# Performance work log

Hardware: AMD Instinct MI355X
Metric: run time of the kernel (lower is better)

## Reference

```python
import jax, jax.numpy as jnp
import numpy as np

H, D, HID = 32, 128, 4096
I = H * D  # inner_dim = 4096
EPS = 1e-6

def l2norm(x):
    n = jnp.sqrt(jnp.sum(x * x, axis=-1, keepdims=True))
    return x / jnp.maximum(n, EPS)

def setup_inputs() -> dict:
    key = jax.random.key(0)
    ks = jax.random.split(key, 13)
    s = 0.02
    return {
        "hidden_states": jax.random.normal(ks[0], (1, 1, HID), jnp.float32),
        "rnn_state": jax.random.normal(ks[1], (1, H, D, D), jnp.float32),
        "conv_state": jax.random.normal(ks[2], (1, 3 * I, 3), jnp.float32),
        "W_qkv": (jax.random.normal(ks[3], (3 * I, HID), jnp.float32) * s),
        "W_z": (jax.random.normal(ks[4], (I, HID), jnp.float32) * s),
        "W_a": (jax.random.normal(ks[5], (H, HID), jnp.float32) * s),
        "W_b": (jax.random.normal(ks[6], (H, HID), jnp.float32) * s),
        "conv_w": (jax.random.normal(ks[7], (3 * I, 4), jnp.float32) * 0.2),  # depthwise kernel [C,1,4] squeezed
        "conv_b": jnp.zeros((3 * I,), jnp.float32),
        "A_log": jnp.log(jax.random.uniform(ks[8], (H,), jnp.float32, 0.5, 2.0)),
        "dt_bias": (jax.random.normal(ks[9], (H,), jnp.float32) * 0.1),
        "norm_w": jnp.ones((D,), jnp.float32),
        "W_out": (jax.random.normal(ks[10], (HID, I), jnp.float32) * s),
    }

def reference(hidden_states, rnn_state, conv_state, W_qkv, W_z, W_a, W_b,
              conv_w, conv_b, A_log, dt_bias, norm_w, W_out):
    B = hidden_states.shape[0]  # == 1 (enforced by original module's view)
    # QKV projection: [B,1,3I]
    qkv = jnp.einsum('bsh,ch->bsc', hidden_states, W_qkv)
    # depthwise causal conv over window of 4 (3 cached + 1 new)
    x_in = jnp.swapaxes(qkv, 1, 2)                      # [B,3I,1]
    conv_input = jnp.concatenate([conv_state, x_in], axis=2)  # [B,3I,4]
    new_conv_state = conv_input[:, :, 1:]
    y = jnp.einsum('bck,ck->bc', conv_input, conv_w) + conv_b
    y = jax.nn.silu(y)                                  # [B,3I]
    q, k, v = jnp.split(y, 3, axis=-1)
    q = q.reshape(B, H, D); k = k.reshape(B, H, D); v = v.reshape(B, H, D)
    # gating projections
    z = jnp.einsum('bsh,ch->bsc', hidden_states, W_z)   # [B,1,I]
    beta = jax.nn.sigmoid(jnp.einsum('bsh,nh->bsn', hidden_states, W_b))[:, 0]  # [B,H]
    a = jnp.einsum('bsh,nh->bsn', hidden_states, W_a)[:, 0]                     # [B,H]
    g = -jnp.exp(A_log) * jax.nn.softplus(a + dt_bias)  # [B,H]
    qn = l2norm(q) * (1.0 / np.sqrt(D))
    kn = l2norm(k)
    # gated delta-rule state update on [B,H,D,D]
    state = rnn_state * jnp.exp(g)[:, :, None, None]
    kv_mem = jnp.einsum('bhde,bhd->bhe', state, kn)
    delta = (v - kv_mem) * beta[..., None]
    state = state + kn[..., None] * delta[:, :, None, :]
    core = jnp.einsum('bhde,bhd->bhe', state, qn)       # [B,H,D]
    # per-head RMSNorm over D (fp32)
    var = jnp.mean(core * core, axis=-1, keepdims=True)
    core = norm_w * (core * jax.lax.rsqrt(var + EPS))
    core = core.reshape(B, 1, I)
    out = jnp.einsum('bsc,hc->bsh', core * jax.nn.silu(z), W_out)
    return out, state, new_conv_state
```

## Files before the change

kernel.cpp:

```cpp
#include <hip/hip_runtime.h>
#include <math.h>

#define HID   4096
#define NH    32
#define D     128
#define I_    4096
#define QKV_ROWS 12288
#define TOTAL_ROWS 16448

#define WS_QKV   0
#define WS_Z     12288
#define WS_AB    16384
#define WS_VEC   16448

typedef float f4 __attribute__((ext_vector_type(4)));

__device__ __forceinline__ float wave_reduce(float x) {
    for (int off = 32; off > 0; off >>= 1) x += __shfl_down(x, off, 64);
    return x;
}

__global__ __launch_bounds__(256) void matvec_all(
    const float* __restrict__ h,
    const float* __restrict__ Wqkv, const float* __restrict__ Wz,
    const float* __restrict__ Wa,   const float* __restrict__ Wb,
    float* __restrict__ ws)
{
    const int wave = threadIdx.x >> 6;
    const int lane = threadIdx.x & 63;
    const int row  = blockIdx.x * 4 + wave;

    const float* W; float* out; int r;
    if (row < QKV_ROWS)          { W = Wqkv; r = row;             out = ws + WS_QKV; }
    else if (row < 16384)        { W = Wz;   r = row - 12288;     out = ws + WS_Z;   }
    else if (row < 16416)        { W = Wa;   r = row - 16384;     out = ws + WS_AB;  }
    else                         { W = Wb;   r = row - 16416;     out = ws + WS_AB + 32; }

    const f4* wrow = (const f4*)(W + (size_t)r * HID);
    const f4* hv   = (const f4*)h;

    float acc = 0.f;
    #pragma unroll
    for (int i = 0; i < 16; ++i) {
        const f4 wv = __builtin_nontemporal_load(wrow + lane + i * 64);
        const f4 hh = hv[lane + i * 64];
        acc = fmaf(wv.x, hh.x, acc);
        acc = fmaf(wv.y, hh.y, acc);
        acc = fmaf(wv.z, hh.z, acc);
        acc = fmaf(wv.w, hh.w, acc);
    }
    acc = wave_reduce(acc);
    if (lane == 0) out[r] = acc;
}

__global__ __launch_bounds__(1024) void head_fused(
    const float* __restrict__ ws_in,
    const float* __restrict__ rnn_state,
    const float* __restrict__ conv_state,
    const float* __restrict__ conv_w,
    const float* __restrict__ conv_b,
    const float* __restrict__ A_log, const float* __restrict__ dt_bias,
    const float* __restrict__ norm_w,
    float* __restrict__ state_out,
    float* __restrict__ ncs_out,
    float* __restrict__ vec_out)
{
    const int hd   = blockIdx.x;
    const int tid  = threadIdx.x;
    const int e    = tid & 127;
    const int dgrp = tid >> 7;
    const int d0   = dgrp * 16;

    __shared__ float sy[3][D];
    __shared__ float skn[D], sqn[D];
    __shared__ float pkv[8][D], pcq[8][D];
    __shared__ float pkq[8];
    __shared__ float sgb[2];
    __shared__ float snrm[2];
    __shared__ float sdelta[D], score[D];
    __shared__ float red[2];

    if (tid < 384) {
        const int j  = tid >> 7;
        const int e2 = tid & 127;
        const int c  = j * I_ + hd * D + e2;
        const float* cs = conv_state + (size_t)c * 3;
        const f4 cw = *(const f4*)(conv_w + (size_t)c * 4);
        const float cs0 = cs[0], cs1 = cs[1], cs2 = cs[2];
        const float x = ws_in[WS_QKV + c];
        float val = fmaf(cs0, cw.x, fmaf(cs1, cw.y,
                    fmaf(cs2, cw.z, fmaf(x, cw.w, conv_b[c]))));
        sy[j][e2] = val / (1.f + expf(-val));
        ncs_out[(size_t)c * 3 + 0] = cs1;
        ncs_out[(size_t)c * 3 + 1] = cs2;
        ncs_out[(size_t)c * 3 + 2] = x;
    }
    if (tid == 0) {
        const float a_ = ws_in[WS_AB + hd];
        const float b_ = ws_in[WS_AB + 32 + hd];
        const float x  = a_ + dt_bias[hd];
        const float sp = fmaxf(x, 0.f) + log1pf(expf(-fabsf(x)));
        sgb[0] = -expf(A_log[hd]) * sp;
        sgb[1] = 1.f / (1.f + expf(-b_));
    }
    __syncthreads();

    if (tid < 128) {
        const int w = tid >> 6, lane = tid & 63;
        const float v0 = sy[w][lane], v1 = sy[w][lane + 64];
        const float ss = wave_reduce(fmaf(v0, v0, v1 * v1));
        if (lane == 0) snrm[w] = ss;
    }
    __syncthreads();
    const float invq = (1.f / fmaxf(sqrtf(snrm[0]), 1e-6f)) * 0.08838834764831843f;
    const float invk =  1.f / fmaxf(sqrtf(snrm[1]), 1e-6f);
    if (tid < 128) {
        sqn[tid] = sy[0][tid] * invq;
        skn[tid] = sy[1][tid] * invk;
    }
    __syncthreads();

    const float eg   = expf(sgb[0]);
    const float beta = sgb[1];
    const float* Sp = rnn_state + (size_t)hd * D * D + (size_t)d0 * D + e;

    float sreg[16];
    #pragma unroll
    for (int j = 0; j < 16; ++j) sreg[j] = Sp[j * D] * eg;

    float kv = 0.f, cq = 0.f;
    #pragma unroll
    for (int j = 0; j < 16; ++j) {
        kv = fmaf(sreg[j], skn[d0 + j], kv);
        cq = fmaf(sreg[j], sqn[d0 + j], cq);
    }
    pkv[dgrp][e] = kv;
    pcq[dgrp][e] = cq;
    if (e == 0) {
        float t = 0.f;
        #pragma unroll
        for (int j = 0; j < 16; ++j) t = fmaf(skn[d0 + j], sqn[d0 + j], t);
        pkq[dgrp] = t;
    }
    __syncthreads();

    if (tid < 128) {
        float kvt = 0.f, cqt = 0.f, kq = 0.f;
        #pragma unroll
        for (int g = 0; g < 8; ++g) {
            kvt += pkv[g][tid];
            cqt += pcq[g][tid];
            kq  += pkq[g];
        }
        const float delta = (sy[2][tid] - kvt) * beta;
        sdelta[tid] = delta;
        const float core = fmaf(delta, kq, cqt);
        score[tid] = core;
        const float c2 = wave_reduce(core * core);
        if ((tid & 63) == 0) red[tid >> 6] = c2;
    }
    __syncthreads();

    float* So = state_out + (size_t)hd * D * D + (size_t)d0 * D + e;
    const float de = sdelta[e];
    #pragma unroll
    for (int j = 0; j < 16; ++j)
        So[j * D] = fmaf(skn[d0 + j], de, sreg[j]);

    if (tid < 128) {
        const float var = (red[0] + red[1]) * (1.f / 128.f);
        const float cn  = norm_w[tid] * score[tid] * rsqrtf(var + 1e-6f);
        const float zz  = ws_in[WS_Z + hd * D + tid];
        vec_out[hd * D + tid] = cn * (zz / (1.f + expf(-zz)));
    }
}

__global__ __launch_bounds__(256) void matvec_out(
    const float* __restrict__ Wout, const float* __restrict__ vec,
    float* __restrict__ out)
{
    const int wave = threadIdx.x >> 6;
    const int lane = threadIdx.x & 63;
    const int row  = blockIdx.x * 4 + wave;

    const f4* wrow = (const f4*)(Wout + (size_t)row * I_);
    const f4* xv   = (const f4*)vec;

    float acc = 0.f;
    #pragma unroll
    for (int i = 0; i < 16; ++i) {
        const f4 wv = __builtin_nontemporal_load(wrow + lane + i * 64);
        const f4 xx = xv[lane + i * 64];
        acc = fmaf(wv.x, xx.x, acc);
        acc = fmaf(wv.y, xx.y, acc);
        acc = fmaf(wv.z, xx.z, acc);
        acc = fmaf(wv.w, xx.w, acc);
    }
    acc = wave_reduce(acc);
    if (lane == 0) out[row] = acc;
}

extern "C" void kernel_launch(void* const* d_in, const int* in_sizes, int n_in,
                              void* d_out, int out_size, void* d_ws, size_t ws_size,
                              hipStream_t stream) {
    const float* hs         = (const float*)d_in[0];
    const float* rnn_state  = (const float*)d_in[1];
    const float* conv_state = (const float*)d_in[2];
    const float* W_qkv      = (const float*)d_in[3];
    const float* W_z        = (const float*)d_in[4];
    const float* W_a        = (const float*)d_in[5];
    const float* W_b        = (const float*)d_in[6];
    const float* conv_w     = (const float*)d_in[7];
    const float* conv_b     = (const float*)d_in[8];
    const float* A_log      = (const float*)d_in[9];
    const float* dt_bias    = (const float*)d_in[10];
    const float* norm_w     = (const float*)d_in[11];
    const float* W_out      = (const float*)d_in[12];

    float* out       = (float*)d_out;
    float* state_out = (float*)d_out + 4096;
    float* ncs_out   = (float*)d_out + 4096 + NH * D * D;
    float* ws        = (float*)d_ws;

    matvec_all<<<TOTAL_ROWS / 4, 256, 0, stream>>>(hs, W_qkv, W_z, W_a, W_b, ws);
    head_fused<<<NH, 1024, 0, stream>>>(ws, rnn_state, conv_state, conv_w, conv_b,
                                        A_log, dt_bias, norm_w,
                                        state_out, ncs_out, ws + WS_VEC);
    matvec_out<<<I_ / 4, 256, 0, stream>>>(W_out, ws + WS_VEC, out);
}
```

Measured before the change: 356.0 us.

## Move conv, gating and silu epilogues into matvec; prefetch rnn_state earlier

The depthwise conv, SiLU, conv-state shift, z-SiLU, softplus decay and sigmoid beta now run as per-row epilogues in the first matvec kernel instead of in the 32-block head kernel. The head kernel then only reads precomputed activations and issues its rnn_state loads at the very start, so those loads overlap the earlier reductions. The aim is to shorten the latency-bound head kernel, which runs on few blocks, at the cost of scattered single-lane epilogue work in the matvec.

```diff
diff --git a/kernel.cpp b/kernel.cpp
--- a/kernel.cpp
+++ b/kernel.cpp
@@ -24,17 +24,22 @@
     const float* __restrict__ h,
     const float* __restrict__ Wqkv, const float* __restrict__ Wz,
     const float* __restrict__ Wa,   const float* __restrict__ Wb,
-    float* __restrict__ ws)
+    const float* __restrict__ conv_state,
+    const float* __restrict__ conv_w,
+    const float* __restrict__ conv_b,
+    const float* __restrict__ A_log, const float* __restrict__ dt_bias,
+    float* __restrict__ ws,
+    float* __restrict__ ncs_out)
 {
     const int wave = threadIdx.x >> 6;
     const int lane = threadIdx.x & 63;
     const int row  = blockIdx.x * 4 + wave;
 
-    const float* W; float* out; int r;
-    if (row < QKV_ROWS)          { W = Wqkv; r = row;             out = ws + WS_QKV; }
-    else if (row < 16384)        { W = Wz;   r = row - 12288;     out = ws + WS_Z;   }
-    else if (row < 16416)        { W = Wa;   r = row - 16384;     out = ws + WS_AB;  }
-    else                         { W = Wb;   r = row - 16416;     out = ws + WS_AB + 32; }
+    const float* W; int r;
+    if (row < QKV_ROWS)          { W = Wqkv; r = row;         }
+    else if (row < 16384)        { W = Wz;   r = row - 12288; }
+    else if (row < 16416)        { W = Wa;   r = row - 16384; }
+    else                         { W = Wb;   r = row - 16416; }
 
     const f4* wrow = (const f4*)(W + (size_t)r * HID);
     const f4* hv   = (const f4*)h;
@@ -50,19 +55,36 @@
         acc = fmaf(wv.w, hh.w, acc);
     }
     acc = wave_reduce(acc);
-    if (lane == 0) out[r] = acc;
+
+    if (lane == 0) {
+        if (row < QKV_ROWS) {
+            const float* cs = conv_state + (size_t)row * 3;
+            const f4 cw = *(const f4*)(conv_w + (size_t)row * 4);
+            const float cs0 = cs[0], cs1 = cs[1], cs2 = cs[2];
+            const float val = fmaf(cs0, cw.x, fmaf(cs1, cw.y,
+                              fmaf(cs2, cw.z, fmaf(acc, cw.w, conv_b[row]))));
+            ws[WS_QKV + row] = val / (1.f + expf(-val));
+            ncs_out[(size_t)row * 3 + 0] = cs1;
+            ncs_out[(size_t)row * 3 + 1] = cs2;
+            ncs_out[(size_t)row * 3 + 2] = acc;
+        } else if (row < 16384) {
+            ws[WS_Z + (row - 12288)] = acc / (1.f + expf(-acc));
+        } else if (row < 16416) {
+            const int rr = row - 16384;
+            const float x  = acc + dt_bias[rr];
+            const float sp = fmaxf(x, 0.f) + log1pf(expf(-fabsf(x)));
+            ws[WS_AB + rr] = expf(-expf(A_log[rr]) * sp);
+        } else {
+            ws[WS_AB + 32 + (row - 16416)] = 1.f / (1.f + expf(-acc));
+        }
+    }
 }
 
 __global__ __launch_bounds__(1024) void head_fused(
     const float* __restrict__ ws_in,
     const float* __restrict__ rnn_state,
-    const float* __restrict__ conv_state,
-    const float* __restrict__ conv_w,
-    const float* __restrict__ conv_b,
-    const float* __restrict__ A_log, const float* __restrict__ dt_bias,
     const float* __restrict__ norm_w,
     float* __restrict__ state_out,
-    float* __restrict__ ncs_out,
     float* __restrict__ vec_out)
 {
     const int hd   = blockIdx.x;
@@ -75,33 +97,19 @@
     __shared__ float skn[D], sqn[D];
     __shared__ float pkv[8][D], pcq[8][D];
     __shared__ float pkq[8];
-    __shared__ float sgb[2];
     __shared__ float snrm[2];
     __shared__ float sdelta[D], score[D];
     __shared__ float red[2];
 
+    const float* Sp = rnn_state + (size_t)hd * D * D + (size_t)d0 * D + e;
+    float sreg[16];
+    #pragma unroll
+    for (int j = 0; j < 16; ++j) sreg[j] = Sp[j * D];
+
     if (tid < 384) {
         const int j  = tid >> 7;
         const int e2 = tid & 127;
-        const int c  = j * I_ + hd * D + e2;
-        const float* cs = conv_state + (size_t)c * 3;
-        const f4 cw = *(const f4*)(conv_w + (size_t)c * 4);
-        const float cs0 = cs[0], cs1 = cs[1], cs2 = cs[2];
-        const float x = ws_in[WS_QKV + c];
-        float val = fmaf(cs0, cw.x, fmaf(cs1, cw.y,
-                    fmaf(cs2, cw.z, fmaf(x, cw.w, conv_b[c]))));
-        sy[j][e2] = val / (1.f + expf(-val));
-        ncs_out[(size_t)c * 3 + 0] = cs1;
-        ncs_out[(size_t)c * 3 + 1] = cs2;
-        ncs_out[(size_t)c * 3 + 2] = x;
-    }
-    if (tid == 0) {
-        const float a_ = ws_in[WS_AB + hd];
-        const float b_ = ws_in[WS_AB + 32 + hd];
-        const float x  = a_ + dt_bias[hd];
-        const float sp = fmaxf(x, 0.f) + log1pf(expf(-fabsf(x)));
-        sgb[0] = -expf(A_log[hd]) * sp;
-        sgb[1] = 1.f / (1.f + expf(-b_));
+        sy[j][e2] = ws_in[WS_QKV + j * I_ + hd * D + e2];
     }
     __syncthreads();
 
@@ -112,25 +120,21 @@
         if (lane == 0) snrm[w] = ss;
     }
     __syncthreads();
-    const float invq = (1.f / fmaxf(sqrtf(snrm[0]), 1e-6f)) * 0.08838834764831843f;
-    const float invk =  1.f / fmaxf(sqrtf(snrm[1]), 1e-6f);
-    if (tid < 128) {
+    if (tid < 128) {
+        const float invq = (1.f / fmaxf(sqrtf(snrm[0]), 1e-6f)) * 0.08838834764831843f;
+        const float invk =  1.f / fmaxf(sqrtf(snrm[1]), 1e-6f);
         sqn[tid] = sy[0][tid] * invq;
         skn[tid] = sy[1][tid] * invk;
     }
     __syncthreads();
 
-    const float eg   = expf(sgb[0]);
-    const float beta = sgb[1];
-    const float* Sp = rnn_state + (size_t)hd * D * D + (size_t)d0 * D + e;
-
-    float sreg[16];
-    #pragma unroll
-    for (int j = 0; j < 16; ++j) sreg[j] = Sp[j * D] * eg;
+    const float eg   = ws_in[WS_AB + hd];
+    const float beta = ws_in[WS_AB + 32 + hd];
 
     float kv = 0.f, cq = 0.f;
     #pragma unroll
     for (int j = 0; j < 16; ++j) {
+        sreg[j] *= eg;
         kv = fmaf(sreg[j], skn[d0 + j], kv);
         cq = fmaf(sreg[j], sqn[d0 + j], cq);
     }
@@ -170,8 +174,7 @@
     if (tid < 128) {
         const float var = (red[0] + red[1]) * (1.f / 128.f);
         const float cn  = norm_w[tid] * score[tid] * rsqrtf(var + 1e-6f);
-        const float zz  = ws_in[WS_Z + hd * D + tid];
-        vec_out[hd * D + tid] = cn * (zz / (1.f + expf(-zz)));
+        vec_out[hd * D + tid] = cn * ws_in[WS_Z + hd * D + tid];
     }
 }
 
@@ -222,9 +225,10 @@
     float* ncs_out   = (float*)d_out + 4096 + NH * D * D;
     float* ws        = (float*)d_ws;
 
-    matvec_all<<<TOTAL_ROWS / 4, 256, 0, stream>>>(hs, W_qkv, W_z, W_a, W_b, ws);
-    head_fused<<<NH, 1024, 0, stream>>>(ws, rnn_state, conv_state, conv_w, conv_b,
-                                        A_log, dt_bias, norm_w,
-                                        state_out, ncs_out, ws + WS_VEC);
+    matvec_all<<<TOTAL_ROWS / 4, 256, 0, stream>>>(hs, W_qkv, W_z, W_a, W_b,
+                                                   conv_state, conv_w, conv_b,
+                                                   A_log, dt_bias, ws, ncs_out);
+    head_fused<<<NH, 1024, 0, stream>>>(ws, rnn_state, norm_w,
+                                        state_out, ws + WS_VEC);
     matvec_out<<<I_ / 4, 256, 0, stream>>>(W_out, ws + WS_VEC, out);
 }
```

Result: no change. 356.5 us (+0.1%).
